# Optimization experiments

Hardware: AMD Instinct MI355X
Metric: run time of the kernel (lower is better)

The kernel has to match this reference:

```python
import jax, jax.numpy as jnp
import numpy as np

EPS = 1e-7          # self.eps[float32]
MIN_NORM = 1e-15
PROJ_EPS = 4e-3     # PoincareBall proj epsilon (float32)
FD_R = 2.0          # args.r
FD_T = 1.0          # args.t
DIS_CLIP = 40.0     # args.dis_mx_clip
ATT_BETA = 0.2      # args.att_beta
# curvature c = 1.0 (self.cur = [1.0, ...]); sqrt_c = 1 so it is folded out below.

def _norm(x):
    return jnp.maximum(jnp.linalg.norm(x, axis=-1, keepdims=True), MIN_NORM)

def expmap0(u):
    n = _norm(u)
    return jnp.tanh(n) * u / n

def proj(x):
    n = _norm(x)
    maxnorm = 1.0 - PROJ_EPS
    return jnp.where(n > maxnorm, x / n * maxnorm, x)

def proj_tan0_exp(u):
    return proj(expmap0(u))

def artanh(x):
    x = jnp.clip(x, -1.0 + EPS, 1.0 - EPS)
    return 0.5 * (jnp.log1p(x) - jnp.log1p(-x))

def mobius_add(x, y):
    x2 = jnp.sum(x * x, -1, keepdims=True)
    y2 = jnp.sum(y * y, -1, keepdims=True)
    xy = jnp.sum(x * y, -1, keepdims=True)
    num = (1.0 + 2.0 * xy + y2) * x + (1.0 - x2) * y
    den = 1.0 + 2.0 * xy + x2 * y2
    return num / jnp.maximum(den, MIN_NORM)

def sqdist(p, q):
    d = 2.0 * artanh(jnp.linalg.norm(mobius_add(-p, q), axis=-1))
    return d * d

def to_klein(x):
    return 2.0 * x / (1.0 + jnp.sum(x * x, -1, keepdims=True))

def lorentz_factor(x):
    return 1.0 / jnp.sqrt(jnp.maximum(1.0 - jnp.sum(x * x, -1), EPS))

def klein_to(x):
    return x / (1.0 + jnp.sqrt(jnp.maximum(1.0 - jnp.sum(x * x, -1, keepdims=True), EPS)))

N_ENTITY, N_REL, DIM = 200000, 32, 64
B, H, M = 1024, 2, 32

def setup_inputs() -> dict:
    key = jax.random.key(0)
    ks = jax.random.split(key, 9)
    return {
        'users': jax.random.randint(ks[0], (B,), 0, 10000),
        'items': jax.random.randint(ks[1], (B,), 0, N_ENTITY),
        'labels': jax.random.randint(ks[2], (B,), 0, 2),
        'mem_h': jax.random.randint(ks[3], (H, B, M), 0, N_ENTITY),
        'mem_r': jax.random.randint(ks[4], (H, B, M), 0, N_REL),
        'mem_t': jax.random.randint(ks[5], (H, B, M), 0, N_ENTITY),
        'entity_emb': 0.05 * jax.random.normal(ks[6], (N_ENTITY, DIM), dtype=jnp.float32),
        'rela_plus_emb': 0.05 * jax.random.normal(ks[7], (N_REL, DIM), dtype=jnp.float32),
        'relation_emb': 0.1 * jax.random.normal(ks[8], (N_REL, DIM * DIM), dtype=jnp.float32),
    }

def reference(users, items, labels, mem_h, mem_r, mem_t,
              entity_emb, rela_plus_emb, relation_emb):
    d = entity_emb.shape[-1]
    item = entity_emb[items]                                  # [B, d]
    h = entity_emb[mem_h]                                     # [H, B, M, d]
    t = entity_emb[mem_t]                                     # [H, B, M, d]
    R = relation_emb[mem_r].reshape(*mem_r.shape, d, d) / 10.0  # [H, B, M, d, d]
    # relation-transform of heads, mapped to the Poincare ball (dropout=eval/identity)
    Rh = proj_tan0_exp(jnp.einsum('hbmij,hbmj->hbmi', R, h))  # [H, B, M, d]
    hyp_item = proj(proj_tan0_exp(item))                      # [B, d] (res = proj(hyp_item))
    dist2 = sqdist(Rh, hyp_item[None, :, None, :])            # [H, B, M]
    att = jnp.exp(-ATT_BETA * dist2 - 0.05)
    kle_t = to_klein(proj_tan0_exp(t))                        # [H, B, M, d]
    p1 = lorentz_factor(kle_t) * att                          # [H, B, M]
    w1 = p1 / jnp.maximum(jnp.sum(p1, -1, keepdims=True), EPS)
    kle_o = jnp.einsum('hbm,hbmd->bhd', w1, kle_t)            # [B, H, d]
    # hop aggregation (one_like_bahop is all-ones)
    p2 = lorentz_factor(kle_o)                                # [B, H]
    w2 = p2 / jnp.maximum(jnp.sum(p2, -1, keepdims=True), EPS)
    o = jnp.einsum('bh,bhd->bd', w2, kle_o)                   # [B, d]
    hyp_o = proj(klein_to(o))
    d2 = sqdist(hyp_o, proj_tan0_exp(item))                   # [B]
    scores = 1.0 / (jnp.exp(jnp.minimum(d2 - FD_R, DIS_CLIP) / FD_T) + 1.0)
    return scores
```

## Files before the change

### kernel.cpp

```cpp
#include <hip/hip_runtime.h>
#include <hip/hip_bf16.h>

#define DIMV 64

static constexpr float F_EPS  = 1e-7f;
static constexpr float F_MINN = 1e-15f;
static constexpr float F_MAXN = 1.0f - 4e-3f;

__device__ __forceinline__ float frcp(float x) { return __builtin_amdgcn_rcpf(x); }
__device__ __forceinline__ float frsq(float x) { return __builtin_amdgcn_rsqf(x); }
__device__ __forceinline__ float tanh_fast(float x) {
    float e = __expf(2.0f * x);
    return 1.0f - 2.0f * frcp(e + 1.0f);
}

__device__ __forceinline__ float wave_sum1(float v) {
#pragma unroll
    for (int off = 32; off > 0; off >>= 1) v += __shfl_xor(v, off, 64);
    return v;
}
__device__ __forceinline__ void wave_sum2(float& a, float& b) {
#pragma unroll
    for (int off = 32; off > 0; off >>= 1) {
        a += __shfl_xor(a, off, 64);
        b += __shfl_xor(b, off, 64);
    }
}

__global__ void k_hist(const int* __restrict__ mr, int n, int* __restrict__ hist) {
    __shared__ int lh[32];
    if (threadIdx.x < 32) lh[threadIdx.x] = 0;
    __syncthreads();
    for (int i = blockIdx.x * blockDim.x + threadIdx.x; i < n; i += gridDim.x * blockDim.x)
        atomicAdd(&lh[mr[i]], 1);
    __syncthreads();
    if (threadIdx.x < 32 && lh[threadIdx.x]) atomicAdd(&hist[threadIdx.x], lh[threadIdx.x]);
}

__global__ void k_scan(const int* __restrict__ hist, int* __restrict__ cursor) {
    if (threadIdx.x == 0) {
        int acc = 0;
        for (int r = 0; r < 32; ++r) { cursor[r] = acc; acc += hist[r]; }
    }
}

__global__ void k_scatter(const int* __restrict__ mr, int n,
                          int* __restrict__ cursor, int* __restrict__ bins) {
    __shared__ int lcnt[32], lbase[32];
    const int tid = threadIdx.x;
    if (tid < 32) lcnt[tid] = 0;
    __syncthreads();
    int idxA[4], rnkA[4], relA[4];
    int cnt = 0;
    int i = blockIdx.x * blockDim.x + tid;
#pragma unroll
    for (int kk = 0; kk < 4; ++kk) {
        if (i < n) {
            int r = mr[i];
            idxA[kk] = i; relA[kk] = r;
            rnkA[kk] = atomicAdd(&lcnt[r], 1);
            cnt = kk + 1;
        }
        i += gridDim.x * blockDim.x;
    }
    __syncthreads();
    if (tid < 32) lbase[tid] = atomicAdd(&cursor[tid], lcnt[tid]);
    __syncthreads();
#pragma unroll
    for (int kk = 0; kk < 4; ++kk)
        if (kk < cnt) bins[lbase[relA[kk]] + rnkA[kk]] = idxA[kk];
}

__global__ __launch_bounds__(256) void k_q(const int* __restrict__ items,
                                           const float* __restrict__ ent,
                                           float* __restrict__ qbuf,
                                           float* __restrict__ y2buf, int B) {
    const int wave = threadIdx.x >> 6, lane = threadIdx.x & 63;
    const int b = blockIdx.x * 4 + wave;
    if (b >= B) return;
    const int it = items[b];
    const float iv = ent[(long)it * DIMV + lane];
    float n2 = wave_sum1(iv * iv);
    float n  = fmaxf(sqrtf(n2), F_MINN);
    float te = tanh_fast(n);
    float s  = (te > F_MAXN) ? F_MAXN * frcp(te) : 1.0f;
    qbuf[(long)b * DIMV + lane] = iv * (te * frcp(n)) * s;
    if (lane == 0) { float qn = te * s; y2buf[b] = qn * qn; }
}

template<int MM, int BB>
__global__ __launch_bounds__(256, 4) void k_att(
        const int*   __restrict__ mem_h,
        const int*   __restrict__ mem_r,
        const float* __restrict__ ent,
        const float* __restrict__ rel,
        const int*   __restrict__ bins,
        const float* __restrict__ qbuf,
        const float* __restrict__ y2buf,
        float*       __restrict__ attbuf,
        int M, int B, int ntask, int per_wave)
{
    const int lane = threadIdx.x & 63;
    const int wid  = blockIdx.x * 4 + (threadIdx.x >> 6);
    const int start = wid * per_wave;

    float Rreg[DIMV];
    int cur_r = -1;

    for (int k = 0; k < per_wave; ++k) {
        const int idx = start + k;
        if (idx >= ntask) return;
        const int t = __builtin_amdgcn_readfirstlane(bins[idx]);
        const int r = __builtin_amdgcn_readfirstlane(mem_r[t]);
        if (r != cur_r) {
            const float4* Rp = (const float4*)(rel + (long)r * (DIMV * DIMV)) + lane * 16;
#pragma unroll
            for (int j = 0; j < 16; ++j) {
                float4 v = Rp[j];
                Rreg[4 * j + 0] = v.x; Rreg[4 * j + 1] = v.y;
                Rreg[4 * j + 2] = v.z; Rreg[4 * j + 3] = v.w;
            }
            cur_r = r;
        }
        const int ih = __builtin_amdgcn_readfirstlane(mem_h[t]);
        const int b  = MM ? ((t >> 5) & (BB - 1))
                          : (int)(((unsigned)t / (unsigned)M) % (unsigned)B);

        const float* hp = ent + (long)ih * DIMV;
        const float  q  = qbuf[(long)b * DIMV + lane];
        const float  y2 = y2buf[b];

        float u0 = 0.f, u1 = 0.f, u2 = 0.f, u3 = 0.f;
#pragma unroll
        for (int j = 0; j < 16; ++j) {
            u0 = fmaf(Rreg[4 * j + 0], hp[4 * j + 0], u0);
            u1 = fmaf(Rreg[4 * j + 1], hp[4 * j + 1], u1);
            u2 = fmaf(Rreg[4 * j + 2], hp[4 * j + 2], u2);
            u3 = fmaf(Rreg[4 * j + 3], hp[4 * j + 3], u3);
        }
        const float u = ((u0 + u1) + (u2 + u3)) * 0.1f;

        float uu = u * u, uq = u * q;
        wave_sum2(uu, uq);

        float nu = fmaxf(sqrtf(uu), F_MINN);
        float te = tanh_fast(nu);
        float sc = (te > F_MAXN) ? F_MAXN * frcp(te) : 1.0f;
        float pn = te * sc;
        float x2 = pn * pn;
        float xy = -(pn * frcp(nu)) * uq;

        float A_  = 1.0f + 2.0f * xy + y2;
        float B_  = 1.0f - x2;
        float nm2 = fmaxf(A_ * A_ * x2 + B_ * B_ * y2 + 2.0f * A_ * B_ * xy, 0.0f);
        float den = fmaxf(1.0f + 2.0f * xy + x2 * y2, 1e-15f);
        float v   = fminf(sqrtf(nm2) * frcp(den), 1.0f - F_EPS);
        float dd  = __logf((1.0f + v) * frcp(1.0f - v));
        float att = __expf(fmaf(-0.2f, dd * dd, -0.05f));

        if (lane == 0) attbuf[t] = att;
    }
}

__global__ __launch_bounds__(256) void k_agg(
        const int*   __restrict__ mem_t,
        const float* __restrict__ ent,
        const float* __restrict__ attbuf,
        const float* __restrict__ qbuf,
        const float* __restrict__ y2buf,
        float*       __restrict__ out,
        int B, int M)
{
    const int b    = blockIdx.x;
    const int wave = threadIdx.x >> 6;
    const int lane = threadIdx.x & 63;
    const int h    = wave >> 1;
    const int mhalf = M >> 1;
    const int mst  = (wave & 1) * mhalf;

    const float q  = qbuf[(long)b * DIMV + lane];
    const float y2 = y2buf[b];

    float accA = 0.0f, accS = 0.0f;
    const long ibase = ((long)h * B + b) * M + mst;

    for (int k = 0; k < mhalf; ++k) {
        const long t  = ibase + k;
        const int itt = __builtin_amdgcn_readfirstlane(mem_t[t]);
        const float av = attbuf[t];
        const float tv = ent[(long)itt * DIMV + lane];
        float tt = wave_sum1(tv * tv);

        float nt  = fmaxf(sqrtf(tt), F_MINN);
        float tte = tanh_fast(nt);
        float ts  = (tte > F_MAXN) ? F_MAXN * frcp(tte) : 1.0f;
        float ptn = tte * ts;
        float a2  = ptn * ptn;
        float i1a = frcp(1.0f + a2);
        float kn2 = 4.0f * a2 * i1a * i1a;
        float lf  = frsq(fmaxf(1.0f - kn2, F_EPS));
        float p1  = lf * av;
        float kfc = 2.0f * ptn * frcp(nt) * i1a;

        accS += p1;
        accA = fmaf(p1 * kfc, tv, accA);
    }

    __shared__ float A_l[4][DIMV];
    __shared__ float S_l[4];
    A_l[wave][lane] = accA;
    if (lane == 0) S_l[wave] = accS;
    __syncthreads();

    if (wave == 0) {
        float k0 = (A_l[0][lane] + A_l[1][lane]) * frcp(fmaxf(S_l[0] + S_l[1], F_EPS));
        float k1 = (A_l[2][lane] + A_l[3][lane]) * frcp(fmaxf(S_l[2] + S_l[3], F_EPS));
        float n0 = k0 * k0, n1 = k1 * k1;
        wave_sum2(n0, n1);
        float p20 = frsq(fmaxf(1.0f - n0, F_EPS));
        float p21 = frsq(fmaxf(1.0f - n1, F_EPS));
        float o   = (p20 * k0 + p21 * k1) * frcp(fmaxf(p20 + p21, F_EPS));

        float oo = o * o, oq = o * q;
        wave_sum2(oo, oq);
        float kd    = 1.0f + sqrtf(fmaxf(1.0f - oo, F_EPS));
        float invkd = frcp(kd);
        float ko2   = oo * invkd * invkd;
        float nk    = fmaxf(sqrtf(ko2), F_MINN);
        float ps    = (nk > F_MAXN) ? F_MAXN * frcp(nk) : 1.0f;
        float x2    = (nk * ps) * (nk * ps);
        float xy    = -(ps * invkd) * oq;

        float A_  = 1.0f + 2.0f * xy + y2;
        float B_  = 1.0f - x2;
        float nm2 = fmaxf(A_ * A_ * x2 + B_ * B_ * y2 + 2.0f * A_ * B_ * xy, 0.0f);
        float den = fmaxf(1.0f + 2.0f * xy + x2 * y2, 1e-15f);
        float v   = fminf(sqrtf(nm2) * frcp(den), 1.0f - F_EPS);
        float dd  = __logf((1.0f + v) * frcp(1.0f - v));
        float d2  = dd * dd;

        float scr = frcp(__expf(fminf(d2 - 2.0f, 40.0f)) + 1.0f);
        if (lane == 0) out[b] = scr;
    }
}

extern "C" void kernel_launch(void* const* d_in, const int* in_sizes, int n_in,
                              void* d_out, int out_size, void* d_ws, size_t ws_size,
                              hipStream_t stream) {
    const int*   items = (const int*)d_in[1];
    const int*   mh    = (const int*)d_in[3];
    const int*   mr    = (const int*)d_in[4];
    const int*   mt    = (const int*)d_in[5];
    const float* ent   = (const float*)d_in[6];
    const float* rel   = (const float*)d_in[8];
    float* out = (float*)d_out;

    const int B = in_sizes[1];
    const int n = in_sizes[3];
    const int M = n / (2 * B);

    float* qbuf   = (float*)d_ws;
    float* y2buf  = qbuf + (size_t)B * DIMV;
    float* attbuf = y2buf + B;
    int*   hist   = (int*)(attbuf + n);
    int*   cursor = hist + 32;
    int*   bins   = cursor + 32;

    hipMemsetAsync(hist, 0, 32 * sizeof(int), stream);
    k_hist<<<dim3(64), dim3(256), 0, stream>>>(mr, n, hist);
    k_scan<<<dim3(1), dim3(64), 0, stream>>>(hist, cursor);
    {
        int g = (n + 1023) / 1024;
        k_scatter<<<dim3(g), dim3(256), 0, stream>>>(mr, n, cursor, bins);
    }
    k_q<<<dim3((B + 3) / 4), dim3(256), 0, stream>>>(items, ent, qbuf, y2buf, B);

    const int per_wave = 16;
    const int g_att = (n + per_wave * 4 - 1) / (per_wave * 4);
    if (M == 32 && B == 1024)
        k_att<32, 1024><<<dim3(g_att), dim3(256), 0, stream>>>(
            mh, mr, ent, rel, bins, qbuf, y2buf, attbuf, M, B, n, per_wave);
    else
        k_att<0, 0><<<dim3(g_att), dim3(256), 0, stream>>>(
            mh, mr, ent, rel, bins, qbuf, y2buf, attbuf, M, B, n, per_wave);

    k_agg<<<dim3(B), dim3(256), 0, stream>>>(mt, ent, attbuf, qbuf, y2buf, out, B, M);
}
```

Before: 165.3 us.

## Move tail-entity norm and Lorentz weight into attention kernel, slim aggregation loop

```diff
diff --git a/kernel.cpp b/kernel.cpp
--- a/kernel.cpp
+++ b/kernel.cpp
@@ -24,6 +24,14 @@
     for (int off = 32; off > 0; off >>= 1) {
         a += __shfl_xor(a, off, 64);
         b += __shfl_xor(b, off, 64);
+    }
+}
+__device__ __forceinline__ void wave_sum3(float& a, float& b, float& c) {
+#pragma unroll
+    for (int off = 32; off > 0; off >>= 1) {
+        a += __shfl_xor(a, off, 64);
+        b += __shfl_xor(b, off, 64);
+        c += __shfl_xor(c, off, 64);
     }
 }
 
@@ -89,22 +97,23 @@
 }
 
 template<int MM, int BB>
-__global__ __launch_bounds__(256, 4) void k_att(
+__global__ __launch_bounds__(256, 4) void k_main(
         const int*   __restrict__ mem_h,
         const int*   __restrict__ mem_r,
+        const int*   __restrict__ mem_t,
         const float* __restrict__ ent,
         const float* __restrict__ rel,
         const int*   __restrict__ bins,
         const float* __restrict__ qbuf,
         const float* __restrict__ y2buf,
-        float*       __restrict__ attbuf,
+        float2*      __restrict__ pkbuf,
         int M, int B, int ntask, int per_wave)
 {
     const int lane = threadIdx.x & 63;
     const int wid  = blockIdx.x * 4 + (threadIdx.x >> 6);
     const int start = wid * per_wave;
 
-    float Rreg[DIMV];
+    float4 r0, r1, r2, r3, r4, r5, r6, r7, r8, r9, r10, r11, r12, r13, r14, r15;
     int cur_r = -1;
 
     for (int k = 0; k < per_wave; ++k) {
@@ -114,34 +123,37 @@
         const int r = __builtin_amdgcn_readfirstlane(mem_r[t]);
         if (r != cur_r) {
             const float4* Rp = (const float4*)(rel + (long)r * (DIMV * DIMV)) + lane * 16;
-#pragma unroll
-            for (int j = 0; j < 16; ++j) {
-                float4 v = Rp[j];
-                Rreg[4 * j + 0] = v.x; Rreg[4 * j + 1] = v.y;
-                Rreg[4 * j + 2] = v.z; Rreg[4 * j + 3] = v.w;
-            }
+            r0  = Rp[0];  r1  = Rp[1];  r2  = Rp[2];  r3  = Rp[3];
+            r4  = Rp[4];  r5  = Rp[5];  r6  = Rp[6];  r7  = Rp[7];
+            r8  = Rp[8];  r9  = Rp[9];  r10 = Rp[10]; r11 = Rp[11];
+            r12 = Rp[12]; r13 = Rp[13]; r14 = Rp[14]; r15 = Rp[15];
             cur_r = r;
         }
-        const int ih = __builtin_amdgcn_readfirstlane(mem_h[t]);
-        const int b  = MM ? ((t >> 5) & (BB - 1))
-                          : (int)(((unsigned)t / (unsigned)M) % (unsigned)B);
+        const int ih  = __builtin_amdgcn_readfirstlane(mem_h[t]);
+        const int itt = __builtin_amdgcn_readfirstlane(mem_t[t]);
+        const int b   = MM ? ((t / MM) & (BB - 1))
+                           : (int)(((unsigned)t / (unsigned)M) % (unsigned)B);
 
         const float* hp = ent + (long)ih * DIMV;
+        const float  tv = ent[(long)itt * DIMV + lane];
         const float  q  = qbuf[(long)b * DIMV + lane];
         const float  y2 = y2buf[b];
 
         float u0 = 0.f, u1 = 0.f, u2 = 0.f, u3 = 0.f;
-#pragma unroll
-        for (int j = 0; j < 16; ++j) {
-            u0 = fmaf(Rreg[4 * j + 0], hp[4 * j + 0], u0);
-            u1 = fmaf(Rreg[4 * j + 1], hp[4 * j + 1], u1);
-            u2 = fmaf(Rreg[4 * j + 2], hp[4 * j + 2], u2);
-            u3 = fmaf(Rreg[4 * j + 3], hp[4 * j + 3], u3);
-        }
+#define STEP(J, RV) \
+        u0 = fmaf(RV.x, hp[4 * (J) + 0], u0); \
+        u1 = fmaf(RV.y, hp[4 * (J) + 1], u1); \
+        u2 = fmaf(RV.z, hp[4 * (J) + 2], u2); \
+        u3 = fmaf(RV.w, hp[4 * (J) + 3], u3);
+        STEP(0, r0)  STEP(1, r1)  STEP(2, r2)  STEP(3, r3)
+        STEP(4, r4)  STEP(5, r5)  STEP(6, r6)  STEP(7, r7)
+        STEP(8, r8)  STEP(9, r9)  STEP(10, r10) STEP(11, r11)
+        STEP(12, r12) STEP(13, r13) STEP(14, r14) STEP(15, r15)
+#undef STEP
         const float u = ((u0 + u1) + (u2 + u3)) * 0.1f;
 
-        float uu = u * u, uq = u * q;
-        wave_sum2(uu, uq);
+        float uu = u * u, uq = u * q, tt = tv * tv;
+        wave_sum3(uu, uq, tt);
 
         float nu = fmaxf(sqrtf(uu), F_MINN);
         float te = tanh_fast(nu);
@@ -158,17 +170,28 @@
         float dd  = __logf((1.0f + v) * frcp(1.0f - v));
         float att = __expf(fmaf(-0.2f, dd * dd, -0.05f));
 
-        if (lane == 0) attbuf[t] = att;
+        float nt  = fmaxf(sqrtf(tt), F_MINN);
+        float tte = tanh_fast(nt);
+        float ts  = (tte > F_MAXN) ? F_MAXN * frcp(tte) : 1.0f;
+        float ptn = tte * ts;
+        float a2  = ptn * ptn;
+        float i1a = frcp(1.0f + a2);
+        float kn2 = 4.0f * a2 * i1a * i1a;
+        float lf  = frsq(fmaxf(1.0f - kn2, F_EPS));
+        float p1  = lf * att;
+        float kfc = 2.0f * ptn * frcp(nt) * i1a;
+
+        if (lane == 0) pkbuf[t] = make_float2(p1, kfc);
     }
 }
 
 __global__ __launch_bounds__(256) void k_agg(
-        const int*   __restrict__ mem_t,
-        const float* __restrict__ ent,
-        const float* __restrict__ attbuf,
-        const float* __restrict__ qbuf,
-        const float* __restrict__ y2buf,
-        float*       __restrict__ out,
+        const int*    __restrict__ mem_t,
+        const float*  __restrict__ ent,
+        const float2* __restrict__ pkbuf,
+        const float*  __restrict__ qbuf,
+        const float*  __restrict__ y2buf,
+        float*        __restrict__ out,
         int B, int M)
 {
     const int b    = blockIdx.x;
@@ -178,32 +201,17 @@
     const int mhalf = M >> 1;
     const int mst  = (wave & 1) * mhalf;
 
-    const float q  = qbuf[(long)b * DIMV + lane];
-    const float y2 = y2buf[b];
-
     float accA = 0.0f, accS = 0.0f;
     const long ibase = ((long)h * B + b) * M + mst;
 
+#pragma unroll 4
     for (int k = 0; k < mhalf; ++k) {
         const long t  = ibase + k;
         const int itt = __builtin_amdgcn_readfirstlane(mem_t[t]);
-        const float av = attbuf[t];
-        const float tv = ent[(long)itt * DIMV + lane];
-        float tt = wave_sum1(tv * tv);
-
-        float nt  = fmaxf(sqrtf(tt), F_MINN);
-        float tte = tanh_fast(nt);
-        float ts  = (tte > F_MAXN) ? F_MAXN * frcp(tte) : 1.0f;
-        float ptn = tte * ts;
-        float a2  = ptn * ptn;
-        float i1a = frcp(1.0f + a2);
-        float kn2 = 4.0f * a2 * i1a * i1a;
-        float lf  = frsq(fmaxf(1.0f - kn2, F_EPS));
-        float p1  = lf * av;
-        float kfc = 2.0f * ptn * frcp(nt) * i1a;
-
-        accS += p1;
-        accA = fmaf(p1 * kfc, tv, accA);
+        const float2 pk = pkbuf[t];
+        const float  tv = ent[(long)itt * DIMV + lane];
+        accS += pk.x;
+        accA = fmaf(pk.x * pk.y, tv, accA);
     }
 
     __shared__ float A_l[4][DIMV];
@@ -213,6 +221,9 @@
     __syncthreads();
 
     if (wave == 0) {
+        const float q  = qbuf[(long)b * DIMV + lane];
+        const float y2 = y2buf[b];
+
         float k0 = (A_l[0][lane] + A_l[1][lane]) * frcp(fmaxf(S_l[0] + S_l[1], F_EPS));
         float k1 = (A_l[2][lane] + A_l[3][lane]) * frcp(fmaxf(S_l[2] + S_l[3], F_EPS));
         float n0 = k0 * k0, n1 = k1 * k1;
@@ -259,12 +270,12 @@
     const int n = in_sizes[3];
     const int M = n / (2 * B);
 
-    float* qbuf   = (float*)d_ws;
-    float* y2buf  = qbuf + (size_t)B * DIMV;
-    float* attbuf = y2buf + B;
-    int*   hist   = (int*)(attbuf + n);
-    int*   cursor = hist + 32;
-    int*   bins   = cursor + 32;
+    float*  qbuf   = (float*)d_ws;
+    float*  y2buf  = qbuf + (size_t)B * DIMV;
+    float2* pkbuf  = (float2*)(y2buf + B);
+    int*    hist   = (int*)((float*)pkbuf + 2 * (size_t)n);
+    int*    cursor = hist + 32;
+    int*    bins   = cursor + 32;
 
     hipMemsetAsync(hist, 0, 32 * sizeof(int), stream);
     k_hist<<<dim3(64), dim3(256), 0, stream>>>(mr, n, hist);
@@ -276,13 +287,13 @@
     k_q<<<dim3((B + 3) / 4), dim3(256), 0, stream>>>(items, ent, qbuf, y2buf, B);
 
     const int per_wave = 16;
-    const int g_att = (n + per_wave * 4 - 1) / (per_wave * 4);
+    const int g_main = (n + per_wave * 4 - 1) / (per_wave * 4);
     if (M == 32 && B == 1024)
-        k_att<32, 1024><<<dim3(g_att), dim3(256), 0, stream>>>(
-            mh, mr, ent, rel, bins, qbuf, y2buf, attbuf, M, B, n, per_wave);
+        k_main<32, 1024><<<dim3(g_main), dim3(256), 0, stream>>>(
+            mh, mr, mt, ent, rel, bins, qbuf, y2buf, pkbuf, M, B, n, per_wave);
     else
-        k_att<0, 0><<<dim3(g_att), dim3(256), 0, stream>>>(
-            mh, mr, ent, rel, bins, qbuf, y2buf, attbuf, M, B, n, per_wave);
-
-    k_agg<<<dim3(B), dim3(256), 0, stream>>>(mt, ent, attbuf, qbuf, y2buf, out, B, M);
-}
+        k_main<0, 0><<<dim3(g_main), dim3(256), 0, stream>>>(
+            mh, mr, mt, ent, rel, bins, qbuf, y2buf, pkbuf, M, B, n, per_wave);
+
+    k_agg<<<dim3(B), dim3(256), 0, stream>>>(mt, ent, pkbuf, qbuf, y2buf, out, B, M);
+}
```

Result: no change. 162.6 us (-1.6%).
